# Kernel tuning notes

Hardware: AMD Instinct MI355X
Metric: run time of the kernel (lower is better)

Reference implementation:

```python
import jax, jax.numpy as jnp
import numpy as np

B, D, NH, H = 32768, 1024, 8, 128
HID = NH * H
K = 4            # conv1d kernel size
EPS = 1e-6
CAP = 15.0       # gate soft cap


def setup_inputs() -> dict:
    key = jax.random.key(0)
    ks = jax.random.split(key, 10)
    w = lambda k, shape: jax.random.normal(k, shape, jnp.float32) * 0.02
    return {
        "inputs": jax.random.normal(ks[0], (B, D), jnp.float32),
        "c": jax.random.normal(ks[1], (B, NH, H), jnp.float32),
        "n": jax.random.uniform(ks[2], (B, NH, H), jnp.float32),
        "m": jax.random.normal(ks[3], (B, NH), jnp.float32),
        "conv_w": w(ks[4], (D, D, K)),        # Conv1d weight [out, in, K]
        "conv_b": jnp.zeros((D,), jnp.float32),
        "z_w": w(ks[5], (HID, D)),            # z_proj (no bias)
        "i_w": w(ks[6], (NH, D)), "i_b": jnp.zeros((NH,), jnp.float32),
        "f_w": w(ks[7], (NH, D)), "f_b": jnp.zeros((NH,), jnp.float32),
        "o_w": w(ks[8], (NH, D)), "o_b": jnp.zeros((NH,), jnp.float32),
        "gn_w": jnp.ones((NH, H), jnp.float32),   # per-head layernorm affine
        "gn_b": jnp.zeros((NH, H), jnp.float32),
        "out_w": w(ks[9], (D, HID)),          # out_proj (no bias)
    }


def _softcap(x):
    return CAP * jnp.tanh(x / CAP)


def reference(inputs, c, n, m, conv_w, conv_b, z_w, i_w, i_b, f_w, f_b,
              o_w, o_b, gn_w, gn_b, out_w):
    # Causal conv on a single timestep: left zero-pad of K-1 means only the
    # last kernel tap touches nonzero data -> x_conv = SiLU(W[:,:,-1] @ x + b).
    x_conv = jax.nn.silu(inputs @ conv_w[:, :, -1].T + conv_b)      # [B, D]

    z = (inputs @ z_w.T).reshape(-1, NH, H)                         # [B, NH, H]
    i_t = _softcap(x_conv @ i_w.T + i_b)                            # [B, NH]
    f_t = _softcap(x_conv @ f_w.T + f_b)
    o_t = _softcap(inputs @ o_w.T + o_b)

    # Stabilized exp gating
    f_log = -jax.nn.softplus(-f_t)                                  # log(sigmoid(f))
    m_new = jnp.maximum(f_log + m, i_t)                             # [B, NH]
    i_g = jnp.exp(i_t - m_new)[..., None]                           # [B, NH, 1]
    f_g = jnp.exp(f_log + m - m_new)[..., None]
    o_g = jax.nn.sigmoid(o_t)[..., None]

    c_new = f_g * c + i_g * z                                       # [B, NH, H]
    n_new = f_g * n + i_g
    h = o_g * (c_new / (n_new + EPS))

    # Per-head layer norm over head_dim with affine params
    mu = jnp.mean(h, axis=-1, keepdims=True)
    var = jnp.var(h, axis=-1, keepdims=True)
    h_norm = (h - mu) * jax.lax.rsqrt(var + EPS) * gn_w + gn_b

    out = h_norm.reshape(-1, HID) @ out_w.T                          # [B, D]
    return (out, c_new, n_new, m_new)
```

## Files before the change

kernel.cpp:

```cpp
#include <hip/hip_runtime.h>
#include <hip/hip_bf16.h>
#include <stdint.h>

#define BQ   32768
#define DD   1024
#define NHH  8
#define HH   128
#define EPSF 1e-6f
#define CAPF 15.0f

typedef unsigned short u16;
typedef short bf16x8 __attribute__((ext_vector_type(8)));
typedef float f32x4  __attribute__((ext_vector_type(4)));

__device__ __forceinline__ float bf2f(u16 v) {
  union { float f; unsigned u; } t; t.u = ((unsigned)v) << 16; return t.f;
}
__device__ __forceinline__ u16 f2bf(float f) {
  union { float f; unsigned u; } t; t.f = f;
  unsigned r = t.u + 0x7fffu + ((t.u >> 16) & 1u);
  return (u16)(r >> 16);
}

#define GLDS16(g, l) \
  __builtin_amdgcn_global_load_lds((const __attribute__((address_space(1))) unsigned int*)(g), \
                                   (__attribute__((address_space(3))) unsigned int*)(l), 16, 0, 0)

template <int EPI>
__global__ __launch_bounds__(256, 2)
void gemm128(const u16* __restrict__ A, const u16* __restrict__ Bt,
             int M, int N, int K,
             const float* __restrict__ bias,
             u16* __restrict__ obf,
             const float* __restrict__ cin, const float* __restrict__ nin,
             const float* __restrict__ gI, const float* __restrict__ gF,
             const float* __restrict__ gO,
             const float* __restrict__ gnw, const float* __restrict__ gnb,
             float* __restrict__ cout, float* __restrict__ nout,
             float* __restrict__ of32)
{
  __shared__ __align__(16) u16 As[128 * 64];
  __shared__ __align__(16) u16 Bs[128 * 64];
  __shared__ float redS[2][128];
  __shared__ float redQ[2][128];
  __shared__ float sgI[128], sgF[128], sgO[128];

  const int t = threadIdx.x;
  const int w = t >> 6;
  const int l = t & 63;

  const int orig = blockIdx.y * 8 + blockIdx.x;
  const int work = ((orig & 7) << 8) | (orig >> 3);
  const int m0 = (work >> 3) * 128;
  const int n0 = (work & 7) * 128;

  const int srow = (w << 5) + (l >> 3);
  const int scol = ((l & 7) ^ (l >> 3)) << 3;
  const u16* gA = A + (size_t)(m0 + srow) * K + scol;
  const u16* gB = Bt + (size_t)(n0 + srow) * K + scol;
  u16* lA = As + (w << 11);
  u16* lB = Bs + (w << 11);

  f32x4 acc[4][4];
#pragma unroll
  for (int i = 0; i < 4; ++i)
#pragma unroll
    for (int j = 0; j < 4; ++j)
      acc[i][j] = (f32x4){0.f, 0.f, 0.f, 0.f};

  const int wm = w & 1, wn = w >> 1;
  const int q = l >> 4, lc = l & 15;
  const int arow = (wm * 64 + lc) * 64;
  const int brow = (wn * 64 + lc) * 64;
  const int sx = (lc & 7) << 3;

  for (int k0 = 0; k0 < K; k0 += 64) {
    __syncthreads();
#pragma unroll
    for (int i = 0; i < 4; ++i) {
      GLDS16(gA + (size_t)(8 * i) * K + k0, lA + i * 512);
      GLDS16(gB + (size_t)(8 * i) * K + k0, lB + i * 512);
    }
    __syncthreads();
#pragma unroll
    for (int kk = 0; kk < 2; ++kk) {
      bf16x8 af[4], bq[4];
      const int ko = ((kk << 5) | (q << 3)) ^ sx;
#pragma unroll
      for (int i = 0; i < 4; ++i) {
        af[i] = *(const bf16x8*)(As + arow + i * 1024 + ko);
        bq[i] = *(const bf16x8*)(Bs + brow + i * 1024 + ko);
      }
#pragma unroll
      for (int i = 0; i < 4; ++i)
#pragma unroll
        for (int j = 0; j < 4; ++j)
          acc[i][j] = __builtin_amdgcn_mfma_f32_16x16x32_bf16(af[i], bq[j], acc[i][j], 0, 0, 0);
    }
  }

  if constexpr (EPI == 1) {
#pragma unroll
    for (int i = 0; i < 4; ++i)
#pragma unroll
      for (int r = 0; r < 4; ++r) {
        size_t row = (size_t)(m0 + wm * 64 + i * 16 + q * 4 + r);
#pragma unroll
        for (int j = 0; j < 4; ++j) {
          int col = n0 + wn * 64 + j * 16 + lc;
          float v = acc[i][j][r] + bias[col];
          float s = v / (1.f + expf(-v));
          obf[row * (size_t)N + col] = f2bf(s);
        }
      }
  }

  if constexpr (EPI == 2) {
    const int head = n0 >> 7;
    if (t < 128) {
      int rr = m0 + t;
      sgI[t] = gI[rr * NHH + head];
      sgF[t] = gF[rr * NHH + head];
      sgO[t] = gO[rr * NHH + head];
    }
    __syncthreads();
#pragma unroll
    for (int i = 0; i < 4; ++i)
#pragma unroll
      for (int r = 0; r < 4; ++r) {
        int rloc = wm * 64 + i * 16 + q * 4 + r;
        size_t grow = (size_t)(m0 + rloc) * (size_t)N;
        float fg = sgF[rloc], ig = sgI[rloc], og = sgO[rloc];
        float s = 0.f, ss = 0.f;
#pragma unroll
        for (int j = 0; j < 4; ++j) {
          int col = n0 + wn * 64 + j * 16 + lc;
          float z  = acc[i][j][r];
          float cv = fg * cin[grow + col] + ig * z;
          float nv = fg * nin[grow + col] + ig;
          cout[grow + col] = cv;
          nout[grow + col] = nv;
          float h = og * cv / (nv + EPSF);
          acc[i][j][r] = h;
          s += h; ss += h * h;
        }
#pragma unroll
        for (int mk = 1; mk < 16; mk <<= 1) {
          s  += __shfl_xor(s,  mk);
          ss += __shfl_xor(ss, mk);
        }
        if (lc == 0) { redS[wn][rloc] = s; redQ[wn][rloc] = ss; }
      }
    __syncthreads();
#pragma unroll
    for (int i = 0; i < 4; ++i)
#pragma unroll
      for (int r = 0; r < 4; ++r) {
        int rloc = wm * 64 + i * 16 + q * 4 + r;
        float s  = redS[0][rloc] + redS[1][rloc];
        float ss = redQ[0][rloc] + redQ[1][rloc];
        float mu  = s * (1.f / 128.f);
        float var = ss * (1.f / 128.f) - mu * mu;
        float rs  = rsqrtf(var + EPSF);
        size_t grow = (size_t)(m0 + rloc) * (size_t)N;
#pragma unroll
        for (int j = 0; j < 4; ++j) {
          int col = n0 + wn * 64 + j * 16 + lc;
          float hn = (acc[i][j][r] - mu) * rs * gnw[col] + gnb[col];
          obf[grow + col] = f2bf(hn);
        }
      }
  }

  if constexpr (EPI == 3) {
#pragma unroll
    for (int i = 0; i < 4; ++i)
#pragma unroll
      for (int r = 0; r < 4; ++r) {
        size_t row = (size_t)(m0 + wm * 64 + i * 16 + q * 4 + r);
#pragma unroll
        for (int j = 0; j < 4; ++j) {
          int col = n0 + wn * 64 + j * 16 + lc;
          of32[row * (size_t)N + col] = acc[i][j][r];
        }
      }
  }
}

__global__ __launch_bounds__(256)
void gates_k(const u16* __restrict__ xbf, const u16* __restrict__ xcbf,
             const u16* __restrict__ wi, const u16* __restrict__ wf,
             const u16* __restrict__ wo,
             const float* __restrict__ ib, const float* __restrict__ fb,
             const float* __restrict__ ob, const float* __restrict__ min_,
             float* __restrict__ gI, float* __restrict__ gF,
             float* __restrict__ gO, float* __restrict__ mout)
{
  const int w = threadIdx.x >> 6, l = threadIdx.x & 63;
  const int row = blockIdx.x * 4 + w;
  const u16* xr  = xbf  + (size_t)row * DD;
  const u16* xcr = xcbf + (size_t)row * DD;
  bf16x8 xa = *(const bf16x8*)(xr + l * 8);
  bf16x8 xb = *(const bf16x8*)(xr + 512 + l * 8);
  bf16x8 ca = *(const bf16x8*)(xcr + l * 8);
  bf16x8 cb = *(const bf16x8*)(xcr + 512 + l * 8);
  float xf[16], cf[16];
#pragma unroll
  for (int j = 0; j < 8; ++j) {
    xf[j] = bf2f((u16)xa[j]); xf[8 + j] = bf2f((u16)xb[j]);
    cf[j] = bf2f((u16)ca[j]); cf[8 + j] = bf2f((u16)cb[j]);
  }
#pragma unroll
  for (int h = 0; h < NHH; ++h) {
    const u16* wip = wi + h * DD;
    const u16* wfp = wf + h * DD;
    const u16* wop = wo + h * DD;
    bf16x8 wia = *(const bf16x8*)(wip + l * 8), wib = *(const bf16x8*)(wip + 512 + l * 8);
    bf16x8 wfa = *(const bf16x8*)(wfp + l * 8), wfb = *(const bf16x8*)(wfp + 512 + l * 8);
    bf16x8 woa = *(const bf16x8*)(wop + l * 8), wob = *(const bf16x8*)(wop + 512 + l * 8);
    float si = 0.f, sf = 0.f, so = 0.f;
#pragma unroll
    for (int j = 0; j < 8; ++j) {
      si += cf[j] * bf2f((u16)wia[j]) + cf[8 + j] * bf2f((u16)wib[j]);
      sf += cf[j] * bf2f((u16)wfa[j]) + cf[8 + j] * bf2f((u16)wfb[j]);
      so += xf[j] * bf2f((u16)woa[j]) + xf[8 + j] * bf2f((u16)wob[j]);
    }
#pragma unroll
    for (int mk = 1; mk < 64; mk <<= 1) {
      si += __shfl_xor(si, mk);
      sf += __shfl_xor(sf, mk);
      so += __shfl_xor(so, mk);
    }
    if (l == 0) {
      float it = CAPF * tanhf((si + ib[h]) / CAPF);
      float ft = CAPF * tanhf((sf + fb[h]) / CAPF);
      float ot = CAPF * tanhf((so + ob[h]) / CAPF);
      float flog = -log1pf(expf(-ft));
      float mo = min_[(size_t)row * NHH + h];
      float mn = fmaxf(flog + mo, it);
      size_t o = (size_t)row * NHH + h;
      gI[o] = expf(it - mn);
      gF[o] = expf(flog + mo - mn);
      gO[o] = 1.f / (1.f + expf(-ot));
      mout[o] = mn;
    }
  }
}

__global__ __launch_bounds__(256)
void cvt_f2b(const float* __restrict__ in, u16* __restrict__ out, int n4) {
  int i = blockIdx.x * 256 + threadIdx.x;
  if (i >= n4) return;
  float4 v = ((const float4*)in)[i];
  ushort4 o;
  o.x = f2bf(v.x); o.y = f2bf(v.y); o.z = f2bf(v.z); o.w = f2bf(v.w);
  ((ushort4*)out)[i] = o;
}

__global__ __launch_bounds__(256)
void cvt_conv(const float* __restrict__ cw, u16* __restrict__ w1) {
  int e = blockIdx.x * 256 + threadIdx.x;
  float4 v = ((const float4*)cw)[e];
  w1[e] = f2bf(v.w);
}

extern "C" void kernel_launch(void* const* d_in, const int* in_sizes, int n_in,
                              void* d_out, int out_size, void* d_ws, size_t ws_size,
                              hipStream_t stream) {
  const float* x_in   = (const float*)d_in[0];
  const float* cst_in = (const float*)d_in[1];
  const float* nst_in = (const float*)d_in[2];
  const float* mst_in = (const float*)d_in[3];
  const float* conv_w = (const float*)d_in[4];
  const float* conv_b = (const float*)d_in[5];
  const float* z_w    = (const float*)d_in[6];
  const float* i_w    = (const float*)d_in[7];
  const float* i_b    = (const float*)d_in[8];
  const float* f_w    = (const float*)d_in[9];
  const float* f_b    = (const float*)d_in[10];
  const float* o_w    = (const float*)d_in[11];
  const float* o_b    = (const float*)d_in[12];
  const float* gn_w   = (const float*)d_in[13];
  const float* gn_b   = (const float*)d_in[14];
  const float* out_w  = (const float*)d_in[15];

  char* ws = (char*)d_ws;
  u16* x_bf  = (u16*)(ws);
  u16* xc_bf = (u16*)(ws + 67108864);
  u16* w1_bf = (u16*)(ws + 134217728);
  u16* zw_bf = (u16*)(ws + 136314880);
  u16* ow_bf = (u16*)(ws + 138412032);
  u16* wi_bf = (u16*)(ws + 140509184);
  u16* wf_bf = (u16*)(ws + 140525568);
  u16* wo_bf = (u16*)(ws + 140541952);
  float* gIv = (float*)(ws + 140558336);
  float* gFv = (float*)(ws + 141606912);
  float* gOv = (float*)(ws + 142655488);

  float* outp  = (float*)d_out;
  float* c_out = outp + (size_t)33554432;
  float* n_out = outp + (size_t)67108864;
  float* m_out = outp + (size_t)100663296;

  cvt_f2b<<<dim3((BQ * DD / 4) / 256), 256, 0, stream>>>(x_in, x_bf, BQ * DD / 4);
  cvt_conv<<<dim3((DD * DD) / 256), 256, 0, stream>>>(conv_w, w1_bf);
  cvt_f2b<<<dim3((DD * DD / 4) / 256), 256, 0, stream>>>(z_w, zw_bf, DD * DD / 4);
  cvt_f2b<<<dim3((DD * DD / 4) / 256), 256, 0, stream>>>(out_w, ow_bf, DD * DD / 4);
  cvt_f2b<<<dim3((NHH * DD / 4 + 255) / 256), 256, 0, stream>>>(i_w, wi_bf, NHH * DD / 4);
  cvt_f2b<<<dim3((NHH * DD / 4 + 255) / 256), 256, 0, stream>>>(f_w, wf_bf, NHH * DD / 4);
  cvt_f2b<<<dim3((NHH * DD / 4 + 255) / 256), 256, 0, stream>>>(o_w, wo_bf, NHH * DD / 4);

  dim3 gg(DD / 128, BQ / 128);

  gemm128<1><<<gg, 256, 0, stream>>>(x_bf, w1_bf, BQ, DD, DD, conv_b, xc_bf,
                                     nullptr, nullptr, nullptr, nullptr, nullptr,
                                     nullptr, nullptr, nullptr, nullptr, nullptr);
  gates_k<<<dim3(BQ / 4), 256, 0, stream>>>(x_bf, xc_bf, wi_bf, wf_bf, wo_bf,
                                            i_b, f_b, o_b, mst_in, gIv, gFv, gOv, m_out);
  gemm128<2><<<gg, 256, 0, stream>>>(x_bf, zw_bf, BQ, DD, DD, nullptr, xc_bf,
                                     cst_in, nst_in, gIv, gFv, gOv, gn_w, gn_b,
                                     c_out, n_out, nullptr);
  gemm128<3><<<gg, 256, 0, stream>>>(xc_bf, ow_bf, BQ, DD, DD, nullptr, nullptr,
                                     nullptr, nullptr, nullptr, nullptr, nullptr,
                                     nullptr, nullptr, nullptr, nullptr, outp);
}
```

Baseline: 1.062 ms.

## Switch GEMMs to 256x256 tiles with double-buffered LDS and interleaved prefetch

Replaces the 128x128 single-buffered GEMM with a 256x256 tile per 512-thread block. The LDS is double-buffered, and the global-to-LDS prefetches for the next K step are split across four MFMA phases, with barriers and s_setprio around each phase. The aim is to hide load latency behind compute and raise arithmetic intensity. The cost is much larger LDS use per block (about 135 KB), which limits occupancy. The gating/layernorm epilogue is also adjusted to cover two heads per tile.

```diff
diff --git a/kernel.cpp b/kernel.cpp
--- a/kernel.cpp
+++ b/kernel.cpp
@@ -27,8 +27,8 @@
                                    (__attribute__((address_space(3))) unsigned int*)(l), 16, 0, 0)
 
 template <int EPI>
-__global__ __launch_bounds__(256, 2)
-void gemm128(const u16* __restrict__ A, const u16* __restrict__ Bt,
+__global__ __launch_bounds__(512, 2)
+void gemm256(const u16* __restrict__ A, const u16* __restrict__ Bt,
              int M, int N, int K,
              const float* __restrict__ bias,
              u16* __restrict__ obf,
@@ -39,72 +39,146 @@
              float* __restrict__ cout, float* __restrict__ nout,
              float* __restrict__ of32)
 {
-  __shared__ __align__(16) u16 As[128 * 64];
-  __shared__ __align__(16) u16 Bs[128 * 64];
-  __shared__ float redS[2][128];
-  __shared__ float redQ[2][128];
-  __shared__ float sgI[128], sgF[128], sgO[128];
+  __shared__ __align__(16) u16 As[2][256 * 64];
+  __shared__ __align__(16) u16 Bs[2][256 * 64];
+  __shared__ float redS[2][2][256];
+  __shared__ float redQ[2][2][256];
+  __shared__ float sgI[2][256], sgF[2][256], sgO[2][256];
 
   const int t = threadIdx.x;
   const int w = t >> 6;
   const int l = t & 63;
 
-  const int orig = blockIdx.y * 8 + blockIdx.x;
-  const int work = ((orig & 7) << 8) | (orig >> 3);
-  const int m0 = (work >> 3) * 128;
-  const int n0 = (work & 7) * 128;
-
-  const int srow = (w << 5) + (l >> 3);
-  const int scol = ((l & 7) ^ (l >> 3)) << 3;
-  const u16* gA = A + (size_t)(m0 + srow) * K + scol;
-  const u16* gB = Bt + (size_t)(n0 + srow) * K + scol;
-  u16* lA = As + (w << 11);
-  u16* lB = Bs + (w << 11);
-
-  f32x4 acc[4][4];
-#pragma unroll
-  for (int i = 0; i < 4; ++i)
+  const int orig = blockIdx.y * 4 + blockIdx.x;
+  const int work = ((orig & 7) << 6) | (orig >> 3);
+  const int m0 = (work >> 2) * 256;
+  const int n0 = (work & 3) * 256;
+
+  const int wm = w & 1, wn = w >> 1;
+  const int q = l >> 4, lc = l & 15;
+
+  const int srow = (w << 3) + (l >> 3);
+  const int sgn  = ((l & 7) ^ (l >> 3)) << 3;
+  const u16* gA = A  + (size_t)(m0 + srow) * K + sgn;
+  const u16* gB = Bt + (size_t)(n0 + srow) * K + sgn;
+
+  f32x4 acc[8][4];
+#pragma unroll
+  for (int i = 0; i < 8; ++i)
 #pragma unroll
     for (int j = 0; j < 4; ++j)
       acc[i][j] = (f32x4){0.f, 0.f, 0.f, 0.f};
 
-  const int wm = w & 1, wn = w >> 1;
-  const int q = l >> 4, lc = l & 15;
-  const int arow = (wm * 64 + lc) * 64;
-  const int brow = (wn * 64 + lc) * 64;
-  const int sx = (lc & 7) << 3;
-
-  for (int k0 = 0; k0 < K; k0 += 64) {
-    __syncthreads();
-#pragma unroll
-    for (int i = 0; i < 4; ++i) {
-      GLDS16(gA + (size_t)(8 * i) * K + k0, lA + i * 512);
-      GLDS16(gB + (size_t)(8 * i) * K + k0, lB + i * 512);
-    }
-    __syncthreads();
-#pragma unroll
-    for (int kk = 0; kk < 2; ++kk) {
-      bf16x8 af[4], bq[4];
-      const int ko = ((kk << 5) | (q << 3)) ^ sx;
-#pragma unroll
-      for (int i = 0; i < 4; ++i) {
-        af[i] = *(const bf16x8*)(As + arow + i * 1024 + ko);
-        bq[i] = *(const bf16x8*)(Bs + brow + i * 1024 + ko);
-      }
-#pragma unroll
-      for (int i = 0; i < 4; ++i)
-#pragma unroll
-        for (int j = 0; j < 4; ++j)
-          acc[i][j] = __builtin_amdgcn_mfma_f32_16x16x32_bf16(af[i], bq[j], acc[i][j], 0, 0, 0);
-    }
+  const int axor  = (lc & 7) << 3;
+  const int abase = (wm * 128 + lc) * 64;
+  const int bbase = (wn * 64  + lc) * 64;
+
+  bf16x8 af[4][2];
+  bf16x8 bq[4][2];
+  const int NT = K >> 6;
+
+#pragma unroll
+  for (int blk = 0; blk < 4; ++blk) {
+    GLDS16(gA + (size_t)(blk * 64) * K, &As[0][(blk * 64 + (w << 3)) * 64]);
+    GLDS16(gB + (size_t)(blk * 64) * K, &Bs[0][(blk * 64 + (w << 3)) * 64]);
+  }
+  asm volatile("s_waitcnt vmcnt(0)" ::: "memory");
+  __builtin_amdgcn_s_barrier();
+
+  for (int tk = 0; tk < NT; ++tk) {
+    const int cb = tk & 1, nb = cb ^ 1;
+    const size_t kn = (size_t)(tk + 1) << 6;
+    const bool pf = (tk + 1 < NT);
+
+#pragma unroll
+    for (int i = 0; i < 4; ++i)
+#pragma unroll
+      for (int kk = 0; kk < 2; ++kk)
+        af[i][kk] = *(const bf16x8*)&As[cb][abase + i * 1024 + (((kk << 5) | (q << 3)) ^ axor)];
+#pragma unroll
+    for (int j = 0; j < 2; ++j)
+#pragma unroll
+      for (int kk = 0; kk < 2; ++kk)
+        bq[j][kk] = *(const bf16x8*)&Bs[cb][bbase + j * 1024 + (((kk << 5) | (q << 3)) ^ axor)];
+    if (pf) {
+      GLDS16(gA + kn,                     &As[nb][(0 * 64 + (w << 3)) * 64]);
+      GLDS16(gA + (size_t)64 * K + kn,    &As[nb][(1 * 64 + (w << 3)) * 64]);
+      GLDS16(gB + kn,                     &Bs[nb][(0 * 64 + (w << 3)) * 64]);
+    }
+    __builtin_amdgcn_s_barrier();
+    __builtin_amdgcn_s_setprio(1);
+#pragma unroll
+    for (int i = 0; i < 4; ++i)
+#pragma unroll
+      for (int j = 0; j < 2; ++j)
+#pragma unroll
+        for (int kk = 0; kk < 2; ++kk)
+          acc[i][j] = __builtin_amdgcn_mfma_f32_16x16x32_bf16(af[i][kk], bq[j][kk], acc[i][j], 0, 0, 0);
+    __builtin_amdgcn_s_setprio(0);
+    __builtin_amdgcn_s_barrier();
+
+#pragma unroll
+    for (int j = 0; j < 2; ++j)
+#pragma unroll
+      for (int kk = 0; kk < 2; ++kk)
+        bq[2 + j][kk] = *(const bf16x8*)&Bs[cb][bbase + (2 + j) * 1024 + (((kk << 5) | (q << 3)) ^ axor)];
+    if (pf) {
+      GLDS16(gA + (size_t)128 * K + kn,   &As[nb][(2 * 64 + (w << 3)) * 64]);
+      GLDS16(gA + (size_t)192 * K + kn,   &As[nb][(3 * 64 + (w << 3)) * 64]);
+      GLDS16(gB + (size_t)64 * K + kn,    &Bs[nb][(1 * 64 + (w << 3)) * 64]);
+    }
+    __builtin_amdgcn_s_barrier();
+    __builtin_amdgcn_s_setprio(1);
+#pragma unroll
+    for (int i = 0; i < 4; ++i)
+#pragma unroll
+      for (int j = 0; j < 2; ++j)
+#pragma unroll
+        for (int kk = 0; kk < 2; ++kk)
+          acc[i][2 + j] = __builtin_amdgcn_mfma_f32_16x16x32_bf16(af[i][kk], bq[2 + j][kk], acc[i][2 + j], 0, 0, 0);
+    __builtin_amdgcn_s_setprio(0);
+    __builtin_amdgcn_s_barrier();
+
+#pragma unroll
+    for (int i = 0; i < 4; ++i)
+#pragma unroll
+      for (int kk = 0; kk < 2; ++kk)
+        af[i][kk] = *(const bf16x8*)&As[cb][abase + (4 + i) * 1024 + (((kk << 5) | (q << 3)) ^ axor)];
+    if (pf) {
+      GLDS16(gB + (size_t)128 * K + kn,   &Bs[nb][(2 * 64 + (w << 3)) * 64]);
+      GLDS16(gB + (size_t)192 * K + kn,   &Bs[nb][(3 * 64 + (w << 3)) * 64]);
+    }
+    __builtin_amdgcn_s_barrier();
+    __builtin_amdgcn_s_setprio(1);
+#pragma unroll
+    for (int i = 0; i < 4; ++i)
+#pragma unroll
+      for (int j = 0; j < 2; ++j)
+#pragma unroll
+        for (int kk = 0; kk < 2; ++kk)
+          acc[4 + i][j] = __builtin_amdgcn_mfma_f32_16x16x32_bf16(af[i][kk], bq[j][kk], acc[4 + i][j], 0, 0, 0);
+    __builtin_amdgcn_s_setprio(0);
+    __builtin_amdgcn_s_barrier();
+
+    __builtin_amdgcn_s_setprio(1);
+#pragma unroll
+    for (int i = 0; i < 4; ++i)
+#pragma unroll
+      for (int j = 0; j < 2; ++j)
+#pragma unroll
+        for (int kk = 0; kk < 2; ++kk)
+          acc[4 + i][2 + j] = __builtin_amdgcn_mfma_f32_16x16x32_bf16(af[i][kk], bq[2 + j][kk], acc[4 + i][2 + j], 0, 0, 0);
+    __builtin_amdgcn_s_setprio(0);
+    asm volatile("s_waitcnt vmcnt(0)" ::: "memory");
+    __builtin_amdgcn_s_barrier();
   }
 
   if constexpr (EPI == 1) {
 #pragma unroll
-    for (int i = 0; i < 4; ++i)
+    for (int i = 0; i < 8; ++i)
 #pragma unroll
       for (int r = 0; r < 4; ++r) {
-        size_t row = (size_t)(m0 + wm * 64 + i * 16 + q * 4 + r);
+        size_t row = (size_t)(m0 + wm * 128 + i * 16 + q * 4 + r);
 #pragma unroll
         for (int j = 0; j < 4; ++j) {
           int col = n0 + wn * 64 + j * 16 + lc;
@@ -116,21 +190,22 @@
   }
 
   if constexpr (EPI == 2) {
-    const int head = n0 >> 7;
-    if (t < 128) {
+    const int hb = n0 >> 7;
+    const int hd = wn >> 1, pi = wn & 1;
+    if (t < 256) {
       int rr = m0 + t;
-      sgI[t] = gI[rr * NHH + head];
-      sgF[t] = gF[rr * NHH + head];
-      sgO[t] = gO[rr * NHH + head];
+      sgI[0][t] = gI[(size_t)rr * NHH + hb];     sgI[1][t] = gI[(size_t)rr * NHH + hb + 1];
+      sgF[0][t] = gF[(size_t)rr * NHH + hb];     sgF[1][t] = gF[(size_t)rr * NHH + hb + 1];
+      sgO[0][t] = gO[(size_t)rr * NHH + hb];     sgO[1][t] = gO[(size_t)rr * NHH + hb + 1];
     }
     __syncthreads();
 #pragma unroll
-    for (int i = 0; i < 4; ++i)
+    for (int i = 0; i < 8; ++i)
 #pragma unroll
       for (int r = 0; r < 4; ++r) {
-        int rloc = wm * 64 + i * 16 + q * 4 + r;
+        int rloc = wm * 128 + i * 16 + q * 4 + r;
         size_t grow = (size_t)(m0 + rloc) * (size_t)N;
-        float fg = sgF[rloc], ig = sgI[rloc], og = sgO[rloc];
+        float fg = sgF[hd][rloc], ig = sgI[hd][rloc], og = sgO[hd][rloc];
         float s = 0.f, ss = 0.f;
 #pragma unroll
         for (int j = 0; j < 4; ++j) {
@@ -149,16 +224,16 @@
           s  += __shfl_xor(s,  mk);
           ss += __shfl_xor(ss, mk);
         }
-        if (lc == 0) { redS[wn][rloc] = s; redQ[wn][rloc] = ss; }
+        if (lc == 0) { redS[pi][hd][rloc] = s; redQ[pi][hd][rloc] = ss; }
       }
     __syncthreads();
 #pragma unroll
-    for (int i = 0; i < 4; ++i)
+    for (int i = 0; i < 8; ++i)
 #pragma unroll
       for (int r = 0; r < 4; ++r) {
-        int rloc = wm * 64 + i * 16 + q * 4 + r;
-        float s  = redS[0][rloc] + redS[1][rloc];
-        float ss = redQ[0][rloc] + redQ[1][rloc];
+        int rloc = wm * 128 + i * 16 + q * 4 + r;
+        float s  = redS[0][hd][rloc] + redS[1][hd][rloc];
+        float ss = redQ[0][hd][rloc] + redQ[1][hd][rloc];
         float mu  = s * (1.f / 128.f);
         float var = ss * (1.f / 128.f) - mu * mu;
         float rs  = rsqrtf(var + EPSF);
@@ -174,10 +249,10 @@
 
   if constexpr (EPI == 3) {
 #pragma unroll
-    for (int i = 0; i < 4; ++i)
+    for (int i = 0; i < 8; ++i)
 #pragma unroll
       for (int r = 0; r < 4; ++r) {
-        size_t row = (size_t)(m0 + wm * 64 + i * 16 + q * 4 + r);
+        size_t row = (size_t)(m0 + wm * 128 + i * 16 + q * 4 + r);
 #pragma unroll
         for (int j = 0; j < 4; ++j) {
           int col = n0 + wn * 64 + j * 16 + lc;
@@ -310,17 +385,17 @@
   cvt_f2b<<<dim3((NHH * DD / 4 + 255) / 256), 256, 0, stream>>>(f_w, wf_bf, NHH * DD / 4);
   cvt_f2b<<<dim3((NHH * DD / 4 + 255) / 256), 256, 0, stream>>>(o_w, wo_bf, NHH * DD / 4);
 
-  dim3 gg(DD / 128, BQ / 128);
-
-  gemm128<1><<<gg, 256, 0, stream>>>(x_bf, w1_bf, BQ, DD, DD, conv_b, xc_bf,
+  dim3 gg(DD / 256, BQ / 256);
+
+  gemm256<1><<<gg, 512, 0, stream>>>(x_bf, w1_bf, BQ, DD, DD, conv_b, xc_bf,
                                      nullptr, nullptr, nullptr, nullptr, nullptr,
                                      nullptr, nullptr, nullptr, nullptr, nullptr);
   gates_k<<<dim3(BQ / 4), 256, 0, stream>>>(x_bf, xc_bf, wi_bf, wf_bf, wo_bf,
                                             i_b, f_b, o_b, mst_in, gIv, gFv, gOv, m_out);
-  gemm128<2><<<gg, 256, 0, stream>>>(x_bf, zw_bf, BQ, DD, DD, nullptr, xc_bf,
+  gemm256<2><<<gg, 512, 0, stream>>>(x_bf, zw_bf, BQ, DD, DD, nullptr, xc_bf,
                                      cst_in, nst_in, gIv, gFv, gOv, gn_w, gn_b,
                                      c_out, n_out, nullptr);
-  gemm128<3><<<gg, 256, 0, stream>>>(xc_bf, ow_bf, BQ, DD, DD, nullptr, nullptr,
+  gemm256<3><<<gg, 512, 0, stream>>>(xc_bf, ow_bf, BQ, DD, DD, nullptr, nullptr,
                                      nullptr, nullptr, nullptr, nullptr, nullptr,
                                      nullptr, nullptr, nullptr, nullptr, outp);
 }
```

Measured after the change: 1.062 ms. About the same (+0.0%).
